# Kernel tuning notes

Hardware: AMD Instinct MI355X
Metric: run time of the kernel (lower is better)

Reference implementation:

```python
import jax, jax.numpy as jnp
import numpy as np

B, S, E, H = 4, 2048, 1024, 16
DK = E // H

def setup_inputs() -> dict:
    key = jax.random.key(0)
    ks = jax.random.split(key, 5)
    scale = 1.0 / np.sqrt(E)
    return {
        "x":  jax.random.normal(ks[0], (B, S, E), dtype=jnp.float32),
        "Wq": jax.random.normal(ks[1], (E, E), dtype=jnp.float32) * scale,
        "Wk": jax.random.normal(ks[2], (E, E), dtype=jnp.float32) * scale,
        "Wv": jax.random.normal(ks[3], (E, E), dtype=jnp.float32) * scale,
        "Wo": jax.random.normal(ks[4], (E, E), dtype=jnp.float32) * scale,
    }

def reference(x, Wq, Wk, Wv, Wo):
    b, s, e = x.shape
    # nn.Linear (no bias): y = x @ W.T
    def split_heads(t):  # (b, s, e) -> (b, H, s, DK)
        return t.reshape(b, s, H, DK).transpose(0, 2, 1, 3)
    Q = split_heads(x @ Wq.T)
    K = split_heads(x @ Wk.T)
    V = split_heads(x @ Wv.T)
    scores = jnp.einsum('bhqd,bhkd->bhqk', Q, K) / jnp.sqrt(jnp.float32(DK))
    attn = jax.nn.softmax(scores, axis=-1)  # dropout p=0.0 -> identity
    ctx = jnp.einsum('bhqk,bhkd->bhqd', attn, V)
    concat = ctx.transpose(0, 2, 1, 3).reshape(b, s, e)
    return concat @ Wo.T
```

## Files before the change

### kernel.cpp

```cpp
#include <hip/hip_runtime.h>


typedef __bf16 bf16x8 __attribute__((ext_vector_type(8)));
typedef __bf16 bf16x4 __attribute__((ext_vector_type(4)));
typedef float floatx4 __attribute__((ext_vector_type(4)));
typedef unsigned int uint2v __attribute__((ext_vector_type(2)));

#define GLOAD_LDS16(gp, lp) __builtin_amdgcn_global_load_lds( \
    (const __attribute__((address_space(1))) unsigned int*)(gp), \
    (__attribute__((address_space(3))) unsigned int*)(lp), 16, 0, 0)

__global__ __launch_bounds__(256) void cvt_all(const float4* __restrict__ x,
                                               const float4* __restrict__ Wq,
                                               const float4* __restrict__ Wk,
                                               const float4* __restrict__ Wv,
                                               const float4* __restrict__ Wo,
                                               bf16x4* __restrict__ xb,
                                               bf16x4* __restrict__ oq, bf16x4* __restrict__ ok,
                                               bf16x4* __restrict__ ov, bf16x4* __restrict__ oo,
                                               float qscale) {
    const int b = blockIdx.x;
    const float4* s;
    bf16x4* d;
    float scale = 1.0f;
    int i;
    if (b < 8192) {
        s = x; d = xb; i = b * 256 + threadIdx.x;
    } else {
        int g = (b - 8192) >> 10;
        s = (g == 0) ? Wq : (g == 1) ? Wk : (g == 2) ? Wv : Wo;
        d = (g == 0) ? oq : (g == 1) ? ok : (g == 2) ? ov : oo;
        if (g == 0) scale = qscale;
        i = ((b - 8192) & 1023) * 256 + threadIdx.x;
    }
    float4 v = s[i];
    bf16x4 o = { (__bf16)(v.x * scale), (__bf16)(v.y * scale),
                 (__bf16)(v.z * scale), (__bf16)(v.w * scale) };
    d[i] = o;
}


__device__ __forceinline__ void gemm_stage(const __bf16* __restrict__ A,
                                           const __bf16* __restrict__ W,
                                           __bf16* Asm, __bf16* Bsm,
                                           int bm, int bn, int k0, int w, int lane) {
#pragma unroll
    for (int j = 0; j < 2; ++j) {
        int base = j * 256 + w * 64;
        int flat = base + lane;
        int c = flat >> 7, r = flat & 127;
        GLOAD_LDS16(A + (size_t)(bm + r) * 1024 + k0 + c * 8, (char*)Asm + base * 16);
    }
#pragma unroll
    for (int j = 0; j < 4; ++j) {
        int base = j * 256 + w * 64;
        int flat = base + lane;
        int c = flat >> 8, r = flat & 255;
        GLOAD_LDS16(W + (size_t)(bn + r) * 1024 + k0 + c * 8, (char*)Bsm + base * 16);
    }
}

__device__ __forceinline__ void gemm_phase(const __bf16* __restrict__ A,
                                           const __bf16* __restrict__ W,
                                           const __bf16* Asm_r, const __bf16* Bsm_r,
                                           __bf16* Asm_s, __bf16* Bsm_s,
                                           int bm, int bn, int ks,
                                           int w, int lane, int quad, int l15,
                                           int wy, int wx,
                                           floatx4 acc[4][8]) {
    gemm_stage(A, W, Asm_s, Bsm_s, bm, bn, ks, w, lane);
    __builtin_amdgcn_sched_barrier(0);
    asm volatile("s_waitcnt vmcnt(6)" ::: "memory");
    __builtin_amdgcn_s_barrier();
    __builtin_amdgcn_sched_barrier(0);

    bf16x8 af[4], bf[8];
#pragma unroll
    for (int mt = 0; mt < 4; ++mt)
        af[mt] = *(const bf16x8*)(Asm_r + (quad * 128 + wy * 64 + mt * 16 + l15) * 8);
#pragma unroll
    for (int nt = 0; nt < 8; ++nt)
        bf[nt] = *(const bf16x8*)(Bsm_r + (quad * 256 + wx * 128 + nt * 16 + l15) * 8);
#pragma unroll
    for (int mt = 0; mt < 4; ++mt)
#pragma unroll
        for (int nt = 0; nt < 8; ++nt)
            acc[mt][nt] = __builtin_amdgcn_mfma_f32_16x16x32_bf16(af[mt], bf[nt],
                                                                  acc[mt][nt], 0, 0, 0);
    __builtin_amdgcn_sched_barrier(0);
    __builtin_amdgcn_s_barrier();
}

__device__ __forceinline__ void gemm_mainloop2(const __bf16* __restrict__ A,
                                               const __bf16* __restrict__ W,
                                               __bf16* SM,
                                               int bm, int bn, int tid,
                                               floatx4 acc[4][8]) {
    const int w = tid >> 6, lane = tid & 63;
    const int quad = lane >> 4, l15 = lane & 15;
    const int wy = w >> 1, wx = w & 1;
    __bf16* Asm0 = SM;
    __bf16* Bsm0 = SM + 4096;
    __bf16* Asm1 = SM + 12288;
    __bf16* Bsm1 = SM + 16384;
#pragma unroll
    for (int i = 0; i < 4; ++i)
#pragma unroll
        for (int j = 0; j < 8; ++j) acc[i][j] = (floatx4){0.f, 0.f, 0.f, 0.f};

    gemm_stage(A, W, Asm0, Bsm0, bm, bn, 0, w, lane);

    for (int k0 = 0; k0 < 1024; k0 += 64) {
        gemm_phase(A, W, Asm0, Bsm0, Asm1, Bsm1, bm, bn, k0 + 32,
                   w, lane, quad, l15, wy, wx, acc);
        gemm_phase(A, W, Asm1, Bsm1, Asm0, Bsm0, bm, bn, k0 + 64,
                   w, lane, quad, l15, wy, wx, acc);
    }
    __syncthreads();
}

__global__ __launch_bounds__(256, 2) void gemm_qkv(const __bf16* __restrict__ A,
                                                   const __bf16* __restrict__ Wqb,
                                                   const __bf16* __restrict__ Wkb,
                                                   const __bf16* __restrict__ Wvb,
                                                   __bf16* __restrict__ Qg,
                                                   __bf16* __restrict__ Kg,
                                                   __bf16* __restrict__ Vtg) {
    __shared__ alignas(16) __bf16 SM[24576];
    const int sel = blockIdx.x >> 2;
    const __bf16* W = (sel == 0) ? Wqb : (sel == 1) ? Wkb : Wvb;
    __bf16* ob = (sel == 0) ? Qg : (sel == 1) ? Kg : Vtg;
    const int bm = blockIdx.y * 128, bn = (blockIdx.x & 3) * 256;
    const int tid = threadIdx.x;
    const int w = tid >> 6, lane = tid & 63;
    const int quad = lane >> 4, l15 = lane & 15;
    const int wy = w >> 1, wx = w & 1;

    floatx4 acc[4][8];
    gemm_mainloop2(A, W, SM, bm, bn, tid, acc);

    float* tb = (float*)SM + w * 272;
    const int rr = lane >> 2, c0 = (lane & 3) * 4;
#pragma unroll
    for (int mt = 0; mt < 4; ++mt)
#pragma unroll
        for (int nt = 0; nt < 8; ++nt) {
            if (sel == 2) {
#pragma unroll
                for (int r = 0; r < 4; ++r) tb[l15 * 17 + quad * 4 + r] = acc[mt][nt][r];
            } else {
#pragma unroll
                for (int r = 0; r < 4; ++r) tb[(quad * 4 + r) * 17 + l15] = acc[mt][nt][r];
            }
            float f0 = tb[rr * 17 + c0 + 0], f1 = tb[rr * 17 + c0 + 1];
            float f2 = tb[rr * 17 + c0 + 2], f3 = tb[rr * 17 + c0 + 3];
            bf16x4 pk = { (__bf16)f0, (__bf16)f1, (__bf16)f2, (__bf16)f3 };
            if (sel <= 1) {
                int m = bm + wy * 64 + mt * 16 + rr;
                int n0 = bn + wx * 128 + nt * 16 + c0;
                int bI = m >> 11, s = m & 2047, h = n0 >> 6, d0 = n0 & 63;
                *(bf16x4*)(ob + ((size_t)(bI * 16 + h) * 2048 + s) * 64 + d0) = pk;
            } else {
                int m0 = bm + wy * 64 + mt * 16 + c0;
                int n = bn + wx * 128 + nt * 16 + rr;
                int bI = m0 >> 11, s0 = m0 & 2047, h = n >> 6, d = n & 63;
                *(bf16x4*)(ob + ((size_t)(bI * 16 + h) * 64 + d) * 2048 + s0) = pk;
            }
        }
}

__global__ __launch_bounds__(256, 2) void gemm_out(const __bf16* __restrict__ A,
                                                   const __bf16* __restrict__ W,
                                                   float* __restrict__ of) {
    __shared__ alignas(16) __bf16 SM[24576];
    const int tid = threadIdx.x;
    const int lane = tid & 63, w = tid >> 6;
    const int quad = lane >> 4, l15 = lane & 15;
    const int wy = w >> 1, wx = w & 1;
    const int bm = blockIdx.y * 128, bn = blockIdx.x * 256;

    floatx4 acc[4][8];
    gemm_mainloop2(A, W, SM, bm, bn, tid, acc);

#pragma unroll
    for (int mt = 0; mt < 4; ++mt)
#pragma unroll
        for (int nt = 0; nt < 8; ++nt)
#pragma unroll
            for (int r = 0; r < 4; ++r) {
                int m = bm + wy * 64 + mt * 16 + quad * 4 + r;
                int n = bn + wx * 128 + nt * 16 + l15;
                of[(size_t)m * 1024 + n] = acc[mt][nt][r];
            }
}


__device__ __forceinline__ void attn_stage_K(const __bf16* __restrict__ Kg,
                                             __bf16* Ks, int bh, int kv0,
                                             int w, int lane) {
#pragma unroll
    for (int j = 0; j < 2; ++j) {
        int base = j * 256 + w * 64;
        int flat = base + lane;
        int c = flat >> 6, r = flat & 63;
        GLOAD_LDS16(Kg + ((size_t)bh * 2048 + kv0 + r) * 64 + c * 8, (char*)Ks + base * 16);
    }
}

__device__ __forceinline__ void attn_stage_V(const __bf16* __restrict__ Vtg,
                                             __bf16* Vs, int bh, int kv0,
                                             int w, int lane) {
#pragma unroll
    for (int j = 0; j < 2; ++j) {
        int base = j * 256 + w * 64;
        int flat = base + lane;
        int c = flat >> 6, r = flat & 63;
        GLOAD_LDS16(Vtg + ((size_t)bh * 64 + r) * 2048 + kv0 + c * 8, (char*)Vs + base * 16);
    }
}

__device__ __forceinline__ void attn_phase(const __bf16* __restrict__ Kg,
                                           const __bf16* __restrict__ Vtg,
                                           const __bf16* Ksr, __bf16* Kss,
                                           __bf16* Vsm,
                                           char* Pw, const bf16x8 qf[2][2],
                                           int bh, int kv_cur, int kv_next,
                                           int w, int lane, int quad, int l15,
                                           float l_p[2], floatx4 o[2][4]) {
    __builtin_amdgcn_s_barrier();
    __builtin_amdgcn_sched_barrier(0);
    attn_stage_V(Vtg, Vsm, bh, kv_cur * 64, w, lane);
    attn_stage_K(Kg, Kss, bh, kv_next * 64, w, lane);
    __builtin_amdgcn_sched_barrier(0);
    asm volatile("s_waitcnt vmcnt(4)" ::: "memory");
    __builtin_amdgcn_s_barrier();
    __builtin_amdgcn_sched_barrier(0);

    floatx4 sa[2][4];
#pragma unroll
    for (int mt = 0; mt < 2; ++mt)
#pragma unroll
        for (int nt = 0; nt < 4; ++nt) sa[mt][nt] = (floatx4){0.f, 0.f, 0.f, 0.f};
#pragma unroll
    for (int nt = 0; nt < 4; ++nt) {
        bf16x8 kb0 = *(const bf16x8*)(Ksr + (quad * 64 + nt * 16 + l15) * 8);
        bf16x8 kb1 = *(const bf16x8*)(Ksr + ((4 + quad) * 64 + nt * 16 + l15) * 8);
#pragma unroll
        for (int mt = 0; mt < 2; ++mt) {
            sa[mt][nt] = __builtin_amdgcn_mfma_f32_16x16x32_bf16(kb0, qf[mt][0],
                                                                sa[mt][nt], 0, 0, 0);
            sa[mt][nt] = __builtin_amdgcn_mfma_f32_16x16x32_bf16(kb1, qf[mt][1],
                                                                sa[mt][nt], 0, 0, 0);
        }
    }

#pragma unroll
    for (int mt = 0; mt < 2; ++mt)
#pragma unroll
        for (int nt = 0; nt < 4; ++nt) {
            float p0 = __builtin_amdgcn_exp2f(sa[mt][nt][0]);
            float p1 = __builtin_amdgcn_exp2f(sa[mt][nt][1]);
            float p2 = __builtin_amdgcn_exp2f(sa[mt][nt][2]);
            float p3 = __builtin_amdgcn_exp2f(sa[mt][nt][3]);
            l_p[mt] += (p0 + p1) + (p2 + p3);
            unsigned u0 = __builtin_bit_cast(unsigned, p0);
            unsigned u1 = __builtin_bit_cast(unsigned, p1);
            unsigned u2 = __builtin_bit_cast(unsigned, p2);
            unsigned u3 = __builtin_bit_cast(unsigned, p3);
            uint2v pk;
            pk.x = __builtin_amdgcn_perm(u1, u0, 0x07060302);
            pk.y = __builtin_amdgcn_perm(u3, u2, 0x07060302);
            *(uint2v*)(Pw + ((nt * 4 + quad) * 32 + mt * 16 + l15) * 8) = pk;
        }

    __builtin_amdgcn_sched_barrier(0);
    asm volatile("s_waitcnt vmcnt(2)" ::: "memory");
    __builtin_amdgcn_s_barrier();
    __builtin_amdgcn_sched_barrier(0);

#pragma unroll
    for (int kk = 0; kk < 2; ++kk) {
        const int c4a = (kk * 4 + quad) * 2;
        bf16x4 lo0 = *(const bf16x4*)(Pw + (c4a * 32 + l15) * 8);
        bf16x4 hi0 = *(const bf16x4*)(Pw + ((c4a + 1) * 32 + l15) * 8);
        bf16x4 lo1 = *(const bf16x4*)(Pw + (c4a * 32 + 16 + l15) * 8);
        bf16x4 hi1 = *(const bf16x4*)(Pw + ((c4a + 1) * 32 + 16 + l15) * 8);
        bf16x8 pa0 = __builtin_shufflevector(lo0, hi0, 0, 1, 2, 3, 4, 5, 6, 7);
        bf16x8 pa1 = __builtin_shufflevector(lo1, hi1, 0, 1, 2, 3, 4, 5, 6, 7);
#pragma unroll
        for (int dt = 0; dt < 4; ++dt) {
            bf16x8 vb = *(const bf16x8*)(Vsm + ((kk * 4 + quad) * 64 + dt * 16 + l15) * 8);
            o[0][dt] = __builtin_amdgcn_mfma_f32_16x16x32_bf16(pa0, vb, o[0][dt], 0, 0, 0);
            o[1][dt] = __builtin_amdgcn_mfma_f32_16x16x32_bf16(pa1, vb, o[1][dt], 0, 0, 0);
        }
    }
    __builtin_amdgcn_sched_barrier(0);
}

__global__ __launch_bounds__(256, 4) void attn_kernel(const __bf16* __restrict__ Qg,
                                                      const __bf16* __restrict__ Kg,
                                                      const __bf16* __restrict__ Vtg,
                                                      __bf16* __restrict__ ctxg) {
    __shared__ alignas(16) __bf16 Ksm0[4096];
    __shared__ alignas(16) __bf16 Ksm1[4096];
    __shared__ alignas(16) __bf16 Vsm[4096];
    __shared__ alignas(16) __bf16 Psm[8192];
    const int tid = threadIdx.x;
    const int w = tid >> 6, lane = tid & 63;
    const int quad = lane >> 4, l15 = lane & 15;

    const int orig = blockIdx.x;
    const int wg = (orig & 7) * 128 + (orig >> 3);
    const int qbase = (wg & 15) * 128;
    const int bh = wg >> 4;

    char* Pw = (char*)Psm + w * 4096;

    bf16x8 qf[2][2];
#pragma unroll
    for (int mt = 0; mt < 2; ++mt) {
        const __bf16* qrow = Qg + ((size_t)bh * 2048 + qbase + w * 32 + mt * 16 + l15) * 64;
        qf[mt][0] = *(const bf16x8*)(qrow + quad * 8);
        qf[mt][1] = *(const bf16x8*)(qrow + 32 + quad * 8);
    }

    float l_p[2] = {0.f, 0.f};
    floatx4 o[2][4];
#pragma unroll
    for (int mt = 0; mt < 2; ++mt)
#pragma unroll
        for (int dt = 0; dt < 4; ++dt) o[mt][dt] = (floatx4){0.f, 0.f, 0.f, 0.f};

    attn_stage_K(Kg, Ksm0, bh, 0, w, lane);

    for (int kv = 0; kv < 32; kv += 2) {
        attn_phase(Kg, Vtg, Ksm0, Ksm1, Vsm, Pw, qf, bh, kv, kv + 1,
                   w, lane, quad, l15, l_p, o);
        attn_phase(Kg, Vtg, Ksm1, Ksm0, Vsm, Pw, qf, bh, kv + 1, kv + 2,
                   w, lane, quad, l15, l_p, o);
    }

    __syncthreads();

    float invr[2][4];
    {
        float inv[2];
#pragma unroll
        for (int mt = 0; mt < 2; ++mt) {
            float t = l_p[mt];
            t += __shfl_xor(t, 16);
            t += __shfl_xor(t, 32);
            inv[mt] = 1.f / t;
        }
#pragma unroll
        for (int mt = 0; mt < 2; ++mt)
#pragma unroll
            for (int r = 0; r < 4; ++r)
                invr[mt][r] = __shfl(inv[mt], quad * 4 + r);
    }

    float* tb = (float*)Ksm0 + w * 272;
    const int bI = bh >> 4, h = bh & 15;
    const int rr = lane >> 2, c0 = (lane & 3) * 4;
#pragma unroll
    for (int mt = 0; mt < 2; ++mt)
#pragma unroll
        for (int dt = 0; dt < 4; ++dt) {
#pragma unroll
            for (int r = 0; r < 4; ++r)
                tb[(quad * 4 + r) * 17 + l15] = o[mt][dt][r] * invr[mt][r];
            float f0 = tb[rr * 17 + c0 + 0], f1 = tb[rr * 17 + c0 + 1];
            float f2 = tb[rr * 17 + c0 + 2], f3 = tb[rr * 17 + c0 + 3];
            bf16x4 pk = { (__bf16)f0, (__bf16)f1, (__bf16)f2, (__bf16)f3 };
            *(bf16x4*)(ctxg + ((size_t)(bI * 2048 + qbase + w * 32 + mt * 16 + rr)) * 1024
                       + h * 64 + dt * 16 + c0) = pk;
        }
}

extern "C" void kernel_launch(void* const* d_in, const int* in_sizes, int n_in,
                              void* d_out, int out_size, void* d_ws, size_t ws_size,
                              hipStream_t stream) {
    const float* x  = (const float*)d_in[0];
    const float* Wq = (const float*)d_in[1];
    const float* Wk = (const float*)d_in[2];
    const float* Wv = (const float*)d_in[3];
    const float* Wo = (const float*)d_in[4];
    float* out = (float*)d_out;
    char* ws = (char*)d_ws;

    __bf16* xb  = (__bf16*)(ws);
    __bf16* wqb = (__bf16*)(ws + (16u << 20));
    __bf16* wkb = (__bf16*)(ws + (18u << 20));
    __bf16* wvb = (__bf16*)(ws + (20u << 20));
    __bf16* wob = (__bf16*)(ws + (22u << 20));
    __bf16* Qg  = (__bf16*)(ws + (24u << 20));
    __bf16* Kg  = (__bf16*)(ws + (40u << 20));
    __bf16* Vtg = (__bf16*)(ws + (56u << 20));
    __bf16* ctx = xb;

    const float qscale = 0.18033688011112042f;

    cvt_all<<<12288, 256, 0, stream>>>((const float4*)x, (const float4*)Wq,
                                       (const float4*)Wk, (const float4*)Wv,
                                       (const float4*)Wo, (bf16x4*)xb,
                                       (bf16x4*)wqb, (bf16x4*)wkb,
                                       (bf16x4*)wvb, (bf16x4*)wob, qscale);

    gemm_qkv<<<dim3(12, 64), 256, 0, stream>>>(xb, wqb, wkb, wvb, Qg, Kg, Vtg);

    attn_kernel<<<1024, 256, 0, stream>>>(Qg, Kg, Vtg, ctx);

    gemm_out<<<dim3(4, 64), 256, 0, stream>>>(ctx, wob, out);
}
```

Before: 300.6 us.

## Enlarge attention query tile per wave and shrink output GEMM tile

The attention kernel now handles 64 query rows per wave (256 per block, 512 blocks), so each K/V tile staged in LDS is reused across twice as many queries. This costs more registers and a larger P buffer, and the occupancy hint drops to 2 blocks per CU. The output projection GEMM switches to 128x128 tiles with a smaller LDS footprint and an occupancy hint of 3 blocks per CU, launching 512 blocks instead of 256 to fill more CUs.

```diff
diff --git a/kernel.cpp b/kernel.cpp
--- a/kernel.cpp
+++ b/kernel.cpp
@@ -119,6 +119,79 @@
     __syncthreads();
 }
 
+__device__ __forceinline__ void gemm_stage_s(const __bf16* __restrict__ A,
+                                             const __bf16* __restrict__ W,
+                                             __bf16* Asm, __bf16* Bsm,
+                                             int bm, int bn, int k0, int w, int lane) {
+#pragma unroll
+    for (int j = 0; j < 2; ++j) {
+        int base = j * 256 + w * 64;
+        int flat = base + lane;
+        int c = flat >> 7, r = flat & 127;
+        GLOAD_LDS16(A + (size_t)(bm + r) * 1024 + k0 + c * 8, (char*)Asm + base * 16);
+        GLOAD_LDS16(W + (size_t)(bn + r) * 1024 + k0 + c * 8, (char*)Bsm + base * 16);
+    }
+}
+
+__device__ __forceinline__ void gemm_phase_s(const __bf16* __restrict__ A,
+                                             const __bf16* __restrict__ W,
+                                             const __bf16* Asm_r, const __bf16* Bsm_r,
+                                             __bf16* Asm_s, __bf16* Bsm_s,
+                                             int bm, int bn, int ks,
+                                             int w, int lane, int quad, int l15,
+                                             int wy, int wx,
+                                             floatx4 acc[4][4]) {
+    gemm_stage_s(A, W, Asm_s, Bsm_s, bm, bn, ks, w, lane);
+    __builtin_amdgcn_sched_barrier(0);
+    asm volatile("s_waitcnt vmcnt(4)" ::: "memory");
+    __builtin_amdgcn_s_barrier();
+    __builtin_amdgcn_sched_barrier(0);
+
+    bf16x8 af[4], bf[4];
+#pragma unroll
+    for (int mt = 0; mt < 4; ++mt)
+        af[mt] = *(const bf16x8*)(Asm_r + (quad * 128 + wy * 64 + mt * 16 + l15) * 8);
+#pragma unroll
+    for (int nt = 0; nt < 4; ++nt)
+        bf[nt] = *(const bf16x8*)(Bsm_r + (quad * 128 + wx * 64 + nt * 16 + l15) * 8);
+#pragma unroll
+    for (int mt = 0; mt < 4; ++mt)
+#pragma unroll
+        for (int nt = 0; nt < 4; ++nt)
+            acc[mt][nt] = __builtin_amdgcn_mfma_f32_16x16x32_bf16(af[mt], bf[nt],
+                                                                  acc[mt][nt], 0, 0, 0);
+    __builtin_amdgcn_sched_barrier(0);
+    __builtin_amdgcn_s_barrier();
+}
+
+__device__ __forceinline__ void gemm_mainloop2s(const __bf16* __restrict__ A,
+                                                const __bf16* __restrict__ W,
+                                                __bf16* SM,
+                                                int bm, int bn, int tid,
+                                                floatx4 acc[4][4]) {
+    const int w = tid >> 6, lane = tid & 63;
+    const int quad = lane >> 4, l15 = lane & 15;
+    const int wy = w >> 1, wx = w & 1;
+    __bf16* Asm0 = SM;
+    __bf16* Bsm0 = SM + 4096;
+    __bf16* Asm1 = SM + 8192;
+    __bf16* Bsm1 = SM + 12288;
+#pragma unroll
+    for (int i = 0; i < 4; ++i)
+#pragma unroll
+        for (int j = 0; j < 4; ++j) acc[i][j] = (floatx4){0.f, 0.f, 0.f, 0.f};
+
+    gemm_stage_s(A, W, Asm0, Bsm0, bm, bn, 0, w, lane);
+
+    for (int k0 = 0; k0 < 1024; k0 += 64) {
+        gemm_phase_s(A, W, Asm0, Bsm0, Asm1, Bsm1, bm, bn, k0 + 32,
+                     w, lane, quad, l15, wy, wx, acc);
+        gemm_phase_s(A, W, Asm1, Bsm1, Asm0, Bsm0, bm, bn, k0 + 64,
+                     w, lane, quad, l15, wy, wx, acc);
+    }
+    __syncthreads();
+}
+
 __global__ __launch_bounds__(256, 2) void gemm_qkv(const __bf16* __restrict__ A,
                                                    const __bf16* __restrict__ Wqb,
                                                    const __bf16* __restrict__ Wkb,
@@ -169,27 +242,27 @@
         }
 }
 
-__global__ __launch_bounds__(256, 2) void gemm_out(const __bf16* __restrict__ A,
+__global__ __launch_bounds__(256, 3) void gemm_out(const __bf16* __restrict__ A,
                                                    const __bf16* __restrict__ W,
                                                    float* __restrict__ of) {
-    __shared__ alignas(16) __bf16 SM[24576];
+    __shared__ alignas(16) __bf16 SM[16384];
     const int tid = threadIdx.x;
     const int lane = tid & 63, w = tid >> 6;
     const int quad = lane >> 4, l15 = lane & 15;
     const int wy = w >> 1, wx = w & 1;
-    const int bm = blockIdx.y * 128, bn = blockIdx.x * 256;
-
-    floatx4 acc[4][8];
-    gemm_mainloop2(A, W, SM, bm, bn, tid, acc);
-
-#pragma unroll
-    for (int mt = 0; mt < 4; ++mt)
-#pragma unroll
-        for (int nt = 0; nt < 8; ++nt)
+    const int bm = blockIdx.y * 128, bn = blockIdx.x * 128;
+
+    floatx4 acc[4][4];
+    gemm_mainloop2s(A, W, SM, bm, bn, tid, acc);
+
+#pragma unroll
+    for (int mt = 0; mt < 4; ++mt)
+#pragma unroll
+        for (int nt = 0; nt < 4; ++nt)
 #pragma unroll
             for (int r = 0; r < 4; ++r) {
                 int m = bm + wy * 64 + mt * 16 + quad * 4 + r;
-                int n = bn + wx * 128 + nt * 16 + l15;
+                int n = bn + wx * 64 + nt * 16 + l15;
                 of[(size_t)m * 1024 + n] = acc[mt][nt][r];
             }
 }
@@ -223,10 +296,10 @@
                                            const __bf16* __restrict__ Vtg,
                                            const __bf16* Ksr, __bf16* Kss,
                                            __bf16* Vsm,
-                                           char* Pw, const bf16x8 qf[2][2],
+                                           char* Pw, const bf16x8 qf[4][2],
                                            int bh, int kv_cur, int kv_next,
                                            int w, int lane, int quad, int l15,
-                                           float l_p[2], floatx4 o[2][4]) {
+                                           float l_p[4], floatx4 o[4][4]) {
     __builtin_amdgcn_s_barrier();
     __builtin_amdgcn_sched_barrier(0);
     attn_stage_V(Vtg, Vsm, bh, kv_cur * 64, w, lane);
@@ -236,9 +309,9 @@
     __builtin_amdgcn_s_barrier();
     __builtin_amdgcn_sched_barrier(0);
 
-    floatx4 sa[2][4];
-#pragma unroll
-    for (int mt = 0; mt < 2; ++mt)
+    floatx4 sa[4][4];
+#pragma unroll
+    for (int mt = 0; mt < 4; ++mt)
 #pragma unroll
         for (int nt = 0; nt < 4; ++nt) sa[mt][nt] = (floatx4){0.f, 0.f, 0.f, 0.f};
 #pragma unroll
@@ -246,7 +319,7 @@
         bf16x8 kb0 = *(const bf16x8*)(Ksr + (quad * 64 + nt * 16 + l15) * 8);
         bf16x8 kb1 = *(const bf16x8*)(Ksr + ((4 + quad) * 64 + nt * 16 + l15) * 8);
 #pragma unroll
-        for (int mt = 0; mt < 2; ++mt) {
+        for (int mt = 0; mt < 4; ++mt) {
             sa[mt][nt] = __builtin_amdgcn_mfma_f32_16x16x32_bf16(kb0, qf[mt][0],
                                                                 sa[mt][nt], 0, 0, 0);
             sa[mt][nt] = __builtin_amdgcn_mfma_f32_16x16x32_bf16(kb1, qf[mt][1],
@@ -255,7 +328,7 @@
     }
 
 #pragma unroll
-    for (int mt = 0; mt < 2; ++mt)
+    for (int mt = 0; mt < 4; ++mt)
 #pragma unroll
         for (int nt = 0; nt < 4; ++nt) {
             float p0 = __builtin_amdgcn_exp2f(sa[mt][nt][0]);
@@ -270,7 +343,7 @@
             uint2v pk;
             pk.x = __builtin_amdgcn_perm(u1, u0, 0x07060302);
             pk.y = __builtin_amdgcn_perm(u3, u2, 0x07060302);
-            *(uint2v*)(Pw + ((nt * 4 + quad) * 32 + mt * 16 + l15) * 8) = pk;
+            *(uint2v*)(Pw + ((nt * 4 + quad) * 64 + mt * 16 + l15) * 8) = pk;
         }
 
     __builtin_amdgcn_sched_barrier(0);
@@ -281,53 +354,56 @@
 #pragma unroll
     for (int kk = 0; kk < 2; ++kk) {
         const int c4a = (kk * 4 + quad) * 2;
-        bf16x4 lo0 = *(const bf16x4*)(Pw + (c4a * 32 + l15) * 8);
-        bf16x4 hi0 = *(const bf16x4*)(Pw + ((c4a + 1) * 32 + l15) * 8);
-        bf16x4 lo1 = *(const bf16x4*)(Pw + (c4a * 32 + 16 + l15) * 8);
-        bf16x4 hi1 = *(const bf16x4*)(Pw + ((c4a + 1) * 32 + 16 + l15) * 8);
-        bf16x8 pa0 = __builtin_shufflevector(lo0, hi0, 0, 1, 2, 3, 4, 5, 6, 7);
-        bf16x8 pa1 = __builtin_shufflevector(lo1, hi1, 0, 1, 2, 3, 4, 5, 6, 7);
+        bf16x8 pa[4];
+#pragma unroll
+        for (int mt = 0; mt < 4; ++mt) {
+            bf16x4 lo = *(const bf16x4*)(Pw + (c4a * 64 + mt * 16 + l15) * 8);
+            bf16x4 hi = *(const bf16x4*)(Pw + ((c4a + 1) * 64 + mt * 16 + l15) * 8);
+            pa[mt] = __builtin_shufflevector(lo, hi, 0, 1, 2, 3, 4, 5, 6, 7);
+        }
 #pragma unroll
         for (int dt = 0; dt < 4; ++dt) {
             bf16x8 vb = *(const bf16x8*)(Vsm + ((kk * 4 + quad) * 64 + dt * 16 + l15) * 8);
-            o[0][dt] = __builtin_amdgcn_mfma_f32_16x16x32_bf16(pa0, vb, o[0][dt], 0, 0, 0);
-            o[1][dt] = __builtin_amdgcn_mfma_f32_16x16x32_bf16(pa1, vb, o[1][dt], 0, 0, 0);
-        }
-    }
-    __builtin_amdgcn_sched_barrier(0);
-}
-
-__global__ __launch_bounds__(256, 4) void attn_kernel(const __bf16* __restrict__ Qg,
+#pragma unroll
+            for (int mt = 0; mt < 4; ++mt)
+                o[mt][dt] = __builtin_amdgcn_mfma_f32_16x16x32_bf16(pa[mt], vb,
+                                                                   o[mt][dt], 0, 0, 0);
+        }
+    }
+    __builtin_amdgcn_sched_barrier(0);
+}
+
+__global__ __launch_bounds__(256, 2) void attn_kernel(const __bf16* __restrict__ Qg,
                                                       const __bf16* __restrict__ Kg,
                                                       const __bf16* __restrict__ Vtg,
                                                       __bf16* __restrict__ ctxg) {
     __shared__ alignas(16) __bf16 Ksm0[4096];
     __shared__ alignas(16) __bf16 Ksm1[4096];
     __shared__ alignas(16) __bf16 Vsm[4096];
-    __shared__ alignas(16) __bf16 Psm[8192];
+    __shared__ alignas(16) __bf16 Psm[16384];
     const int tid = threadIdx.x;
     const int w = tid >> 6, lane = tid & 63;
     const int quad = lane >> 4, l15 = lane & 15;
 
     const int orig = blockIdx.x;
-    const int wg = (orig & 7) * 128 + (orig >> 3);
-    const int qbase = (wg & 15) * 128;
-    const int bh = wg >> 4;
-
-    char* Pw = (char*)Psm + w * 4096;
-
-    bf16x8 qf[2][2];
-#pragma unroll
-    for (int mt = 0; mt < 2; ++mt) {
-        const __bf16* qrow = Qg + ((size_t)bh * 2048 + qbase + w * 32 + mt * 16 + l15) * 64;
+    const int wg = (orig & 7) * 64 + (orig >> 3);
+    const int qbase = (wg & 7) * 256;
+    const int bh = wg >> 3;
+
+    char* Pw = (char*)Psm + w * 8192;
+
+    bf16x8 qf[4][2];
+#pragma unroll
+    for (int mt = 0; mt < 4; ++mt) {
+        const __bf16* qrow = Qg + ((size_t)bh * 2048 + qbase + w * 64 + mt * 16 + l15) * 64;
         qf[mt][0] = *(const bf16x8*)(qrow + quad * 8);
         qf[mt][1] = *(const bf16x8*)(qrow + 32 + quad * 8);
     }
 
-    float l_p[2] = {0.f, 0.f};
-    floatx4 o[2][4];
-#pragma unroll
-    for (int mt = 0; mt < 2; ++mt)
+    float l_p[4] = {0.f, 0.f, 0.f, 0.f};
+    floatx4 o[4][4];
+#pragma unroll
+    for (int mt = 0; mt < 4; ++mt)
 #pragma unroll
         for (int dt = 0; dt < 4; ++dt) o[mt][dt] = (floatx4){0.f, 0.f, 0.f, 0.f};
 
@@ -342,18 +418,18 @@
 
     __syncthreads();
 
-    float invr[2][4];
+    float invr[4][4];
     {
-        float inv[2];
-#pragma unroll
-        for (int mt = 0; mt < 2; ++mt) {
+        float inv[4];
+#pragma unroll
+        for (int mt = 0; mt < 4; ++mt) {
             float t = l_p[mt];
             t += __shfl_xor(t, 16);
             t += __shfl_xor(t, 32);
             inv[mt] = 1.f / t;
         }
 #pragma unroll
-        for (int mt = 0; mt < 2; ++mt)
+        for (int mt = 0; mt < 4; ++mt)
 #pragma unroll
             for (int r = 0; r < 4; ++r)
                 invr[mt][r] = __shfl(inv[mt], quad * 4 + r);
@@ -363,7 +439,7 @@
     const int bI = bh >> 4, h = bh & 15;
     const int rr = lane >> 2, c0 = (lane & 3) * 4;
 #pragma unroll
-    for (int mt = 0; mt < 2; ++mt)
+    for (int mt = 0; mt < 4; ++mt)
 #pragma unroll
         for (int dt = 0; dt < 4; ++dt) {
 #pragma unroll
@@ -372,7 +448,7 @@
             float f0 = tb[rr * 17 + c0 + 0], f1 = tb[rr * 17 + c0 + 1];
             float f2 = tb[rr * 17 + c0 + 2], f3 = tb[rr * 17 + c0 + 3];
             bf16x4 pk = { (__bf16)f0, (__bf16)f1, (__bf16)f2, (__bf16)f3 };
-            *(bf16x4*)(ctxg + ((size_t)(bI * 2048 + qbase + w * 32 + mt * 16 + rr)) * 1024
+            *(bf16x4*)(ctxg + ((size_t)(bI * 2048 + qbase + w * 64 + mt * 16 + rr)) * 1024
                        + h * 64 + dt * 16 + c0) = pk;
         }
 }
@@ -408,7 +484,7 @@
 
     gemm_qkv<<<dim3(12, 64), 256, 0, stream>>>(xb, wqb, wkb, wvb, Qg, Kg, Vtg);
 
-    attn_kernel<<<1024, 256, 0, stream>>>(Qg, Kg, Vtg, ctx);
-
-    gemm_out<<<dim3(4, 64), 256, 0, stream>>>(ctx, wob, out);
-}
+    attn_kernel<<<512, 256, 0, stream>>>(Qg, Kg, Vtg, ctx);
+
+    gemm_out<<<dim3(8, 64), 256, 0, stream>>>(ctx, wob, out);
+}
```

New measurement: 303.4 us. No clear change (+0.9%).

## Retile projection GEMMs to 256x256 blocks with 512 threads and K=64 stages

Applied to the files above, without the earlier changes.

Both projection GEMMs move from 128x256 tiles with 4 waves to 256x256 tiles with 8 waves. Each stage now loads K=64 into a unified 64KB A+B buffer, double-buffered in 128KB of LDS, with two MFMA k-substeps per stage. The goal is more data reuse per loaded byte and fewer barriers per unit of K. In exchange, the grid shrinks: 384 blocks for QKV and 128 for the output projection. The large LDS footprint likely limits each CU to one block, which risks underfilling the device and causing tail imbalance.

```diff
diff --git a/kernel.cpp b/kernel.cpp
--- a/kernel.cpp
+++ b/kernel.cpp
@@ -42,155 +42,148 @@
 
 __device__ __forceinline__ void gemm_stage(const __bf16* __restrict__ A,
                                            const __bf16* __restrict__ W,
-                                           __bf16* Asm, __bf16* Bsm,
+                                           char* dbuf,
                                            int bm, int bn, int k0, int w, int lane) {
 #pragma unroll
-    for (int j = 0; j < 2; ++j) {
-        int base = j * 256 + w * 64;
+    for (int j = 0; j < 4; ++j) {
+        int base = j * 512 + w * 64;
         int flat = base + lane;
-        int c = flat >> 7, r = flat & 127;
-        GLOAD_LDS16(A + (size_t)(bm + r) * 1024 + k0 + c * 8, (char*)Asm + base * 16);
-    }
-#pragma unroll
-    for (int j = 0; j < 4; ++j) {
-        int base = j * 256 + w * 64;
-        int flat = base + lane;
-        int c = flat >> 8, r = flat & 255;
-        GLOAD_LDS16(W + (size_t)(bn + r) * 1024 + k0 + c * 8, (char*)Bsm + base * 16);
+        int kc = flat >> 8, r = flat & 255;
+        GLOAD_LDS16(A + (size_t)(bm + r) * 1024 + k0 + kc * 8, dbuf + base * 16);
+        GLOAD_LDS16(W + (size_t)(bn + r) * 1024 + k0 + kc * 8, dbuf + 32768 + base * 16);
     }
 }
 
 __device__ __forceinline__ void gemm_phase(const __bf16* __restrict__ A,
                                            const __bf16* __restrict__ W,
-                                           const __bf16* Asm_r, const __bf16* Bsm_r,
-                                           __bf16* Asm_s, __bf16* Bsm_s,
+                                           const char* dr, char* ds,
                                            int bm, int bn, int ks,
                                            int w, int lane, int quad, int l15,
-                                           int wy, int wx,
-                                           floatx4 acc[4][8]) {
-    gemm_stage(A, W, Asm_s, Bsm_s, bm, bn, ks, w, lane);
-    __builtin_amdgcn_sched_barrier(0);
-    asm volatile("s_waitcnt vmcnt(6)" ::: "memory");
+                                           int wr, int wc,
+                                           floatx4 acc[8][4]) {
+    gemm_stage(A, W, ds, bm, bn, ks, w, lane);
+    __builtin_amdgcn_sched_barrier(0);
+    asm volatile("s_waitcnt vmcnt(8)" ::: "memory");
     __builtin_amdgcn_s_barrier();
     __builtin_amdgcn_sched_barrier(0);
 
-    bf16x8 af[4], bf[8];
-#pragma unroll
-    for (int mt = 0; mt < 4; ++mt)
-        af[mt] = *(const bf16x8*)(Asm_r + (quad * 128 + wy * 64 + mt * 16 + l15) * 8);
-#pragma unroll
-    for (int nt = 0; nt < 8; ++nt)
-        bf[nt] = *(const bf16x8*)(Bsm_r + (quad * 256 + wx * 128 + nt * 16 + l15) * 8);
-#pragma unroll
-    for (int mt = 0; mt < 4; ++mt)
-#pragma unroll
-        for (int nt = 0; nt < 8; ++nt)
-            acc[mt][nt] = __builtin_amdgcn_mfma_f32_16x16x32_bf16(af[mt], bf[nt],
-                                                                  acc[mt][nt], 0, 0, 0);
+#pragma unroll
+    for (int ksub = 0; ksub < 2; ++ksub) {
+        const int kc = ksub * 4 + quad;
+        bf16x8 af[8], bf[4];
+#pragma unroll
+        for (int mtg = 0; mtg < 8; ++mtg)
+            af[mtg] = *(const bf16x8*)(dr + (kc * 256 + wr * 128 + mtg * 16 + l15) * 16);
+#pragma unroll
+        for (int nt = 0; nt < 4; ++nt)
+            bf[nt] = *(const bf16x8*)(dr + 32768 + (kc * 256 + wc * 64 + nt * 16 + l15) * 16);
+#pragma unroll
+        for (int mtg = 0; mtg < 8; ++mtg)
+#pragma unroll
+            for (int nt = 0; nt < 4; ++nt)
+                acc[mtg][nt] = __builtin_amdgcn_mfma_f32_16x16x32_bf16(af[mtg], bf[nt],
+                                                                       acc[mtg][nt], 0, 0, 0);
+    }
     __builtin_amdgcn_sched_barrier(0);
     __builtin_amdgcn_s_barrier();
 }
 
-__device__ __forceinline__ void gemm_mainloop2(const __bf16* __restrict__ A,
-                                               const __bf16* __restrict__ W,
-                                               __bf16* SM,
-                                               int bm, int bn, int tid,
-                                               floatx4 acc[4][8]) {
+__device__ __forceinline__ void gemm_mainloop(const __bf16* __restrict__ A,
+                                              const __bf16* __restrict__ W,
+                                              char* SM,
+                                              int bm, int bn, int tid,
+                                              floatx4 acc[8][4]) {
     const int w = tid >> 6, lane = tid & 63;
     const int quad = lane >> 4, l15 = lane & 15;
-    const int wy = w >> 1, wx = w & 1;
-    __bf16* Asm0 = SM;
-    __bf16* Bsm0 = SM + 4096;
-    __bf16* Asm1 = SM + 12288;
-    __bf16* Bsm1 = SM + 16384;
-#pragma unroll
-    for (int i = 0; i < 4; ++i)
-#pragma unroll
-        for (int j = 0; j < 8; ++j) acc[i][j] = (floatx4){0.f, 0.f, 0.f, 0.f};
-
-    gemm_stage(A, W, Asm0, Bsm0, bm, bn, 0, w, lane);
-
-    for (int k0 = 0; k0 < 1024; k0 += 64) {
-        gemm_phase(A, W, Asm0, Bsm0, Asm1, Bsm1, bm, bn, k0 + 32,
-                   w, lane, quad, l15, wy, wx, acc);
-        gemm_phase(A, W, Asm1, Bsm1, Asm0, Bsm0, bm, bn, k0 + 64,
-                   w, lane, quad, l15, wy, wx, acc);
+    const int wr = w >> 2, wc = w & 3;
+    char* d0 = SM;
+    char* d1 = SM + 65536;
+#pragma unroll
+    for (int i = 0; i < 8; ++i)
+#pragma unroll
+        for (int j = 0; j < 4; ++j) acc[i][j] = (floatx4){0.f, 0.f, 0.f, 0.f};
+
+    gemm_stage(A, W, d0, bm, bn, 0, w, lane);
+
+    for (int k0 = 0; k0 < 1024; k0 += 128) {
+        gemm_phase(A, W, d0, d1, bm, bn, k0 + 64, w, lane, quad, l15, wr, wc, acc);
+        gemm_phase(A, W, d1, d0, bm, bn, k0 + 128, w, lane, quad, l15, wr, wc, acc);
     }
     __syncthreads();
 }
 
-__global__ __launch_bounds__(256, 2) void gemm_qkv(const __bf16* __restrict__ A,
+__global__ __launch_bounds__(512, 2) void gemm_qkv(const __bf16* __restrict__ A,
                                                    const __bf16* __restrict__ Wqb,
                                                    const __bf16* __restrict__ Wkb,
                                                    const __bf16* __restrict__ Wvb,
                                                    __bf16* __restrict__ Qg,
                                                    __bf16* __restrict__ Kg,
                                                    __bf16* __restrict__ Vtg) {
-    __shared__ alignas(16) __bf16 SM[24576];
+    __shared__ alignas(16) char SM[131072];
     const int sel = blockIdx.x >> 2;
     const __bf16* W = (sel == 0) ? Wqb : (sel == 1) ? Wkb : Wvb;
     __bf16* ob = (sel == 0) ? Qg : (sel == 1) ? Kg : Vtg;
-    const int bm = blockIdx.y * 128, bn = (blockIdx.x & 3) * 256;
+    const int bm = blockIdx.y * 256, bn = (blockIdx.x & 3) * 256;
     const int tid = threadIdx.x;
     const int w = tid >> 6, lane = tid & 63;
     const int quad = lane >> 4, l15 = lane & 15;
-    const int wy = w >> 1, wx = w & 1;
-
-    floatx4 acc[4][8];
-    gemm_mainloop2(A, W, SM, bm, bn, tid, acc);
+    const int wr = w >> 2, wc = w & 3;
+
+    floatx4 acc[8][4];
+    gemm_mainloop(A, W, SM, bm, bn, tid, acc);
 
     float* tb = (float*)SM + w * 272;
     const int rr = lane >> 2, c0 = (lane & 3) * 4;
 #pragma unroll
-    for (int mt = 0; mt < 4; ++mt)
-#pragma unroll
-        for (int nt = 0; nt < 8; ++nt) {
+    for (int mtg = 0; mtg < 8; ++mtg)
+#pragma unroll
+        for (int nt = 0; nt < 4; ++nt) {
             if (sel == 2) {
 #pragma unroll
-                for (int r = 0; r < 4; ++r) tb[l15 * 17 + quad * 4 + r] = acc[mt][nt][r];
+                for (int r = 0; r < 4; ++r) tb[l15 * 17 + quad * 4 + r] = acc[mtg][nt][r];
             } else {
 #pragma unroll
-                for (int r = 0; r < 4; ++r) tb[(quad * 4 + r) * 17 + l15] = acc[mt][nt][r];
+                for (int r = 0; r < 4; ++r) tb[(quad * 4 + r) * 17 + l15] = acc[mtg][nt][r];
             }
             float f0 = tb[rr * 17 + c0 + 0], f1 = tb[rr * 17 + c0 + 1];
             float f2 = tb[rr * 17 + c0 + 2], f3 = tb[rr * 17 + c0 + 3];
             bf16x4 pk = { (__bf16)f0, (__bf16)f1, (__bf16)f2, (__bf16)f3 };
             if (sel <= 1) {
-                int m = bm + wy * 64 + mt * 16 + rr;
-                int n0 = bn + wx * 128 + nt * 16 + c0;
+                int m = bm + wr * 128 + mtg * 16 + rr;
+                int n0 = bn + wc * 64 + nt * 16 + c0;
                 int bI = m >> 11, s = m & 2047, h = n0 >> 6, d0 = n0 & 63;
                 *(bf16x4*)(ob + ((size_t)(bI * 16 + h) * 2048 + s) * 64 + d0) = pk;
             } else {
-                int m0 = bm + wy * 64 + mt * 16 + c0;
-                int n = bn + wx * 128 + nt * 16 + rr;
+                int m0 = bm + wr * 128 + mtg * 16 + c0;
+                int n = bn + wc * 64 + nt * 16 + rr;
                 int bI = m0 >> 11, s0 = m0 & 2047, h = n >> 6, d = n & 63;
                 *(bf16x4*)(ob + ((size_t)(bI * 16 + h) * 64 + d) * 2048 + s0) = pk;
             }
         }
 }
 
-__global__ __launch_bounds__(256, 2) void gemm_out(const __bf16* __restrict__ A,
+__global__ __launch_bounds__(512, 2) void gemm_out(const __bf16* __restrict__ A,
                                                    const __bf16* __restrict__ W,
                                                    float* __restrict__ of) {
-    __shared__ alignas(16) __bf16 SM[24576];
+    __shared__ alignas(16) char SM[131072];
     const int tid = threadIdx.x;
     const int lane = tid & 63, w = tid >> 6;
     const int quad = lane >> 4, l15 = lane & 15;
-    const int wy = w >> 1, wx = w & 1;
-    const int bm = blockIdx.y * 128, bn = blockIdx.x * 256;
-
-    floatx4 acc[4][8];
-    gemm_mainloop2(A, W, SM, bm, bn, tid, acc);
-
-#pragma unroll
-    for (int mt = 0; mt < 4; ++mt)
-#pragma unroll
-        for (int nt = 0; nt < 8; ++nt)
+    const int wr = w >> 2, wc = w & 3;
+    const int bm = blockIdx.y * 256, bn = blockIdx.x * 256;
+
+    floatx4 acc[8][4];
+    gemm_mainloop(A, W, SM, bm, bn, tid, acc);
+
+#pragma unroll
+    for (int mtg = 0; mtg < 8; ++mtg)
+#pragma unroll
+        for (int nt = 0; nt < 4; ++nt)
 #pragma unroll
             for (int r = 0; r < 4; ++r) {
-                int m = bm + wy * 64 + mt * 16 + quad * 4 + r;
-                int n = bn + wx * 128 + nt * 16 + l15;
-                of[(size_t)m * 1024 + n] = acc[mt][nt][r];
+                int m = bm + wr * 128 + mtg * 16 + quad * 4 + r;
+                int n = bn + wc * 64 + nt * 16 + l15;
+                of[(size_t)m * 1024 + n] = acc[mtg][nt][r];
             }
 }
 
@@ -406,9 +399,9 @@
                                        (bf16x4*)wqb, (bf16x4*)wkb,
                                        (bf16x4*)wvb, (bf16x4*)wob, qscale);
 
-    gemm_qkv<<<dim3(12, 64), 256, 0, stream>>>(xb, wqb, wkb, wvb, Qg, Kg, Vtg);
+    gemm_qkv<<<dim3(12, 32), 512, 0, stream>>>(xb, wqb, wkb, wvb, Qg, Kg, Vtg);
 
     attn_kernel<<<1024, 256, 0, stream>>>(Qg, Kg, Vtg, ctx);
 
-    gemm_out<<<dim3(4, 64), 256, 0, stream>>>(ctx, wob, out);
-}
+    gemm_out<<<dim3(4, 32), 512, 0, stream>>>(ctx, wob, out);
+}
```

Result: slower. 357.4 us (+18.9%).
